# Optimization experiments

Measured on AMD Instinct MI355X. Metric: run time of the kernel, lower is better.

## Reference

```python
import jax, jax.numpy as jnp
import numpy as np

B, SD, SE = 4, 2048, 2048
HID, HID_ = 300, 512
N_HEADS = 8


def setup_inputs() -> dict:
    key = jax.random.key(0)
    ks = jax.random.split(key, 7)
    en = jax.random.normal(ks[0], (B, SE, HID), dtype=jnp.float32)
    de = jax.random.normal(ks[1], (B, SD, HID), dtype=jnp.float32)
    mask = jax.random.randint(ks[2], (1, 1, SD, SE), 0, 2).astype(jnp.bool_)
    WQ = jax.random.normal(ks[3], (HID, HID_), dtype=jnp.float32)
    WK = jax.random.normal(ks[4], (HID, HID_), dtype=jnp.float32)
    WV = jax.random.normal(ks[5], (HID, HID_), dtype=jnp.float32)
    WO = jax.random.normal(ks[6], (HID_, HID), dtype=jnp.float32)
    return {"en": en, "de": de, "mask": mask, "WQ": WQ, "WK": WK, "WV": WV, "WO": WO}


def reference(en, de, mask, WQ, WK, WV, WO):
    # Faithful to the torch module (dropout in eval mode => identity).
    d_k = de.shape[-1]  # NOTE: original scales by sqrt(hidden_dim)=sqrt(300), not head_dim
    b_d, s_d = de.shape[0], de.shape[1]
    b_e, s_e = en.shape[0], en.shape[1]
    # head axis is the LAST axis of the reshape (size 8), exactly as the original view/permute
    q = jnp.transpose((de @ WQ).reshape(b_d, s_d, -1, N_HEADS), (3, 0, 1, 2))  # [8,B,Sd,64]
    k = jnp.transpose((en @ WK).reshape(b_e, s_e, -1, N_HEADS), (3, 0, 2, 1))  # [8,B,64,Se]
    v = jnp.transpose((en @ WV).reshape(b_e, s_e, -1, N_HEADS), (3, 0, 1, 2))  # [8,B,Se,64]
    e = jnp.matmul(q, k) / jnp.sqrt(jnp.asarray(d_k, dtype=q.dtype))           # [8,B,Sd,Se]
    e = jnp.where(mask, jnp.asarray(-1e9, dtype=e.dtype), e)
    alpha = jax.nn.softmax(e, axis=3)
    head3 = jnp.matmul(alpha, v)                                               # [8,B,Sd,64]
    # torch.cat((head3[0],...,head3[7]), 2) == move head axis into feature concat order
    a = jnp.concatenate([head3[h] for h in range(N_HEADS)], axis=2)            # [B,Sd,512]
    return a @ WO                                                              # [B,Sd,300]
```

## Files before the change

kernel.cpp:

```cpp
#include <hip/hip_runtime.h>
#include <hip/hip_bf16.h>
#include <math.h>

#define B_      4
#define SD_     2048
#define SE_     2048
#define HIDIN   300
#define HIDMID  512
#define NH      8
#define DH      64
#define ESZ     ((size_t)4194304)
#define BUFB    24576

typedef __attribute__((ext_vector_type(8))) short          s16x8;
typedef __attribute__((ext_vector_type(8))) unsigned short u16x8;
typedef __attribute__((ext_vector_type(4))) unsigned short u16x4;
typedef __attribute__((ext_vector_type(4))) float          f32x4;

#define MFMA16 __builtin_amdgcn_mfma_f32_16x16x32_bf16

#define QSCALE  0.0832940411f
#define NEGL   -1.4426950e9f
#define DEFER_THR 24.0f

__device__ __forceinline__ unsigned short f2bf(float f) {
    unsigned int u = __float_as_uint(f);
    u += 0x7fffu + ((u >> 16) & 1u);
    return (unsigned short)(u >> 16);
}
__device__ __forceinline__ float bf2f(unsigned short s) {
    return __uint_as_float((unsigned int)s << 16);
}
__device__ __forceinline__ void gload16(const void* g, void* l) {
    __builtin_amdgcn_global_load_lds(
        (const __attribute__((address_space(1))) void*)g,
        (__attribute__((address_space(3))) void*)l, 16, 0, 0);
}

#define OF_QH   ((size_t)0)
#define OF_QL   (ESZ)
#define OF_KH   (2*ESZ)
#define OF_KL   (3*ESZ)
#define OF_VT   (4*ESZ)
#define OF_CA   (5*ESZ)
#define OF_CW   (OF_CA + 10485760)
#define OF_WOT  (OF_CW + 983040)

__global__ __launch_bounds__(256) void bias_kernel(const int* __restrict__ mask,
                                                   unsigned int* __restrict__ BiasT)
{
    const int idx = blockIdx.x * 256 + threadIdx.x;
    const int q = idx >> 5, tile = idx & 31;
    const int* __restrict__ mrow = mask + (size_t)q * SE_ + tile * 64;
    const unsigned int NEGB = (unsigned int)f2bf(NEGL);
    const int qblk = q >> 4, qlo = q & 15;
#pragma unroll
    for (int g = 0; g < 4; ++g) {
        unsigned int w[8];
#pragma unroll
        for (int sub = 0; sub < 4; ++sub) {
            const int4 mm = *(const int4*)(mrow + sub * 16 + g * 4);
            w[sub * 2]     = (mm.x ? NEGB : 0u) | ((mm.y ? NEGB : 0u) << 16);
            w[sub * 2 + 1] = (mm.z ? NEGB : 0u) | ((mm.w ? NEGB : 0u) << 16);
        }
        unsigned int* dst = BiasT +
            ((((size_t)qblk * 32 + tile) * 4 + g) * 16 + qlo) * 8;
        *(uint4*)dst       = make_uint4(w[0], w[1], w[2], w[3]);
        *(uint4*)(dst + 4) = make_uint4(w[4], w[5], w[6], w[7]);
    }
}

__global__ __launch_bounds__(256) void convA_kernel(
    const float* __restrict__ de, const float* __restrict__ en,
    unsigned short* __restrict__ CA)
{
    const int idx = blockIdx.x * 256 + threadIdx.x;
    const int mat = blockIdx.y;
    const float* __restrict__ A = mat ? en : de;
    unsigned short* __restrict__ H = CA + (size_t)mat * 5242880;
    unsigned short* __restrict__ L = H + 2621440;
    const int row = idx / 10, ch = idx - row * 10;
    float v[32];
    if (ch < 9) {
#pragma unroll
        for (int i = 0; i < 8; ++i) {
            const float4 f = *(const float4*)(A + (size_t)row * 300 + ch * 32 + i * 4);
            v[i*4+0] = f.x; v[i*4+1] = f.y; v[i*4+2] = f.z; v[i*4+3] = f.w;
        }
    } else {
#pragma unroll
        for (int i = 0; i < 32; ++i) {
            const int k = 288 + i;
            v[i] = (k < 300) ? A[(size_t)row * 300 + k] : 0.f;
        }
    }
    const int r128 = row & 127;
    const int xr = (r128 >> 1) & 3;
    const size_t tb = ((size_t)(row >> 7) * 10 + ch) * 4096 + r128 * 32;
#pragma unroll
    for (int sub = 0; sub < 4; ++sub) {
        const int slot = sub ^ xr;
        u16x8 hv, lv;
#pragma unroll
        for (int e = 0; e < 8; ++e) {
            const float f = v[sub * 8 + e];
            const unsigned short h = f2bf(f);
            hv[e] = h; lv[e] = f2bf(f - bf2f(h));
        }
        *(u16x8*)(H + tb + slot * 8) = hv;
        *(u16x8*)(L + tb + slot * 8) = lv;
    }
}

__global__ __launch_bounds__(256) void convW_kernel(
    const float* __restrict__ WQ, const float* __restrict__ WK,
    const float* __restrict__ WV, const float* __restrict__ WO,
    unsigned short* __restrict__ CW, unsigned short* __restrict__ WOT)
{
    const int idx = blockIdx.x * 256 + threadIdx.x;
    if (idx < 122880) {
        const int which = idx / 40960;
        const int rem = idx - which * 40960;
        const int k = rem >> 7;
        const int n0 = (rem & 127) * 4;
        const float* __restrict__ W = which == 0 ? WQ : (which == 1 ? WK : WV);
        unsigned short* __restrict__ H = CW + (size_t)which * 327680;
        unsigned short* __restrict__ L = H + 163840;
        const float sc = (which == 0) ? QSCALE : 1.f;
        float4 w = make_float4(0.f, 0.f, 0.f, 0.f);
        if (k < 300) w = *(const float4*)(W + (size_t)k * 512 + n0);
        const float wv4[4] = {w.x * sc, w.y * sc, w.z * sc, w.w * sc};
        const int ch = k >> 5, kk = k & 31;
#pragma unroll
        for (int j = 0; j < 4; ++j) {
            const int n = n0 + j, ntile = n >> 7, nr = n & 127;
            const size_t o = ((size_t)(ntile * 10 + ch) * 128 + nr) * 32
                           + (((kk >> 3) ^ ((nr >> 1) & 3)) << 3) + (kk & 7);
            const unsigned short h = f2bf(wv4[j]);
            H[o] = h; L[o] = f2bf(wv4[j] - bf2f(h));
        }
    } else {
        const int idx2 = idx - 122880;
        const int k = idx2 / 96, n4 = idx2 - k * 96;
        const int n0 = n4 * 4;
        float4 w = make_float4(0.f, 0.f, 0.f, 0.f);
        if (n0 < 300) w = *(const float4*)(WO + (size_t)k * 300 + n0);
        const float wv4[4] = {w.x, w.y, w.z, w.w};
        const int ch = k >> 5, kk = k & 31;
#pragma unroll
        for (int j = 0; j < 4; ++j) {
            const int n = n0 + j, ntile = n >> 7, nr = n & 127;
            const size_t o = ((size_t)(ntile * 16 + ch) * 128 + nr) * 32
                           + (((kk >> 3) ^ ((nr >> 1) & 3)) << 3) + (kk & 7);
            WOT[o] = f2bf(wv4[j]);
        }
    }
}

__global__ __launch_bounds__(256) void proj_mfma_kernel(
    const unsigned short* __restrict__ CA, const unsigned short* __restrict__ CW,
    unsigned short* __restrict__ Qh, unsigned short* __restrict__ Ql,
    unsigned short* __restrict__ KhT, unsigned short* __restrict__ KlT,
    unsigned short* __restrict__ VtT)
{
    const int stile = blockIdx.x, jtile = blockIdx.y, which = blockIdx.z;
    const int tid = threadIdx.x, wv = tid >> 6, lane = tid & 63;
    const int li = lane & 15, g = lane >> 4;
    const int wr = wv >> 1, wc = wv & 1;

    __shared__ __align__(16) char LBp[65536];

    const unsigned short* __restrict__ pAh =
        CA + (size_t)(which ? 1 : 0) * 5242880 + (size_t)stile * 40960 + tid * 8;
    const unsigned short* __restrict__ pAl = pAh + 2621440;
    const unsigned short* __restrict__ pWh =
        CW + (size_t)which * 327680 + (size_t)jtile * 40960 + tid * 8;
    const unsigned short* __restrict__ pWl = pWh + 163840;

#define STAGEP(ch, bofs) {                                                    \
        char* db = LBp + (bofs) + wv * 1024;                                  \
        const size_t co = (size_t)(ch) * 4096;                                \
        gload16(pAh + co,        db);                                         \
        gload16(pAh + co + 2048, db + 4096);                                  \
        gload16(pAl + co,        db + 8192);                                  \
        gload16(pAl + co + 2048, db + 12288);                                 \
        gload16(pWh + co,        db + 16384);                                 \
        gload16(pWh + co + 2048, db + 20480);                                 \
        gload16(pWl + co,        db + 24576);                                 \
        gload16(pWl + co + 2048, db + 28672);                                 \
    }

    int offA[4], offW[4];
#pragma unroll
    for (int ssub = 0; ssub < 4; ++ssub) {
        const int r = wr * 64 + ssub * 16 + li;
        offA[ssub] = r * 64 + ((g ^ ((r >> 1) & 3)) << 4);
    }
#pragma unroll
    for (int jsub = 0; jsub < 4; ++jsub) {
        const int n = wc * 64 + jsub * 16 + li;
        offW[jsub] = n * 64 + ((g ^ ((n >> 1) & 3)) << 4);
    }

    f32x4 acc[4][4];
#pragma unroll
    for (int i = 0; i < 4; ++i)
#pragma unroll
        for (int j = 0; j < 4; ++j) acc[i][j] = (f32x4){0.f, 0.f, 0.f, 0.f};

    STAGEP(0, 0)
    __syncthreads();

#pragma unroll 1
    for (int ch = 0; ch < 10; ++ch) {
        const int bofs = (ch & 1) * 32768;
        if (ch < 9) STAGEP(ch + 1, bofs ^ 32768)
        const char* bp = LBp + bofs;
        s16x8 ah[4], al[4], wh[4], wl[4];
#pragma unroll
        for (int ssub = 0; ssub < 4; ++ssub) {
            ah[ssub] = *(const s16x8*)(bp + offA[ssub]);
            al[ssub] = *(const s16x8*)(bp + 8192 + offA[ssub]);
        }
#pragma unroll
        for (int jsub = 0; jsub < 4; ++jsub) {
            wh[jsub] = *(const s16x8*)(bp + 16384 + offW[jsub]);
            wl[jsub] = *(const s16x8*)(bp + 24576 + offW[jsub]);
        }
        __builtin_amdgcn_s_setprio(1);
#pragma unroll
        for (int ssub = 0; ssub < 4; ++ssub)
#pragma unroll
            for (int jsub = 0; jsub < 4; ++jsub) {
                acc[ssub][jsub] = MFMA16(ah[ssub], wh[jsub], acc[ssub][jsub], 0, 0, 0);
                acc[ssub][jsub] = MFMA16(ah[ssub], wl[jsub], acc[ssub][jsub], 0, 0, 0);
                acc[ssub][jsub] = MFMA16(al[ssub], wh[jsub], acc[ssub][jsub], 0, 0, 0);
            }
        __builtin_amdgcn_s_setprio(0);
        __syncthreads();
    }
#undef STAGEP

    const int jgbase = jtile * 128 + wc * 64 + li;
    const int sbase0 = stile * 128 + wr * 64 + 4 * g;
#pragma unroll
    for (int jsub = 0; jsub < 4; ++jsub) {
        const int jgg = jgbase + jsub * 16;
        const int d = jgg >> 3, hh = jgg & 7;
#pragma unroll
        for (int ssub = 0; ssub < 4; ++ssub) {
            const f32x4 v = acc[ssub][jsub];
            const int sg0 = sbase0 + ssub * 16;
            const int bbv = sg0 >> 11;
            const int bhn = bbv * 8 + hh;
            const int sl0 = sg0 & 2047;
            if (which == 0) {
                const size_t o = ((size_t)bhn * 2048 + sl0) * 64 + d;
#pragma unroll
                for (int r = 0; r < 4; ++r) {
                    const float val = v[r];
                    const unsigned short hi = f2bf(val);
                    Qh[o + r * 64] = hi;
                    Ql[o + r * 64] = f2bf(val - bf2f(hi));
                }
            } else if (which == 1) {
                const int tile = sl0 >> 6, tt0 = sl0 & 63;
                const size_t tb = ((size_t)(bhn * 32 + tile)) << 12;
#pragma unroll
                for (int r = 0; r < 4; ++r) {
                    const int tt = tt0 + r;
                    const size_t o = tb + tt * 64 + (((d >> 3) ^ (tt & 7)) << 3) + (d & 7);
                    const float val = v[r];
                    const unsigned short hi = f2bf(val);
                    KhT[o] = hi;
                    KlT[o] = f2bf(val - bf2f(hi));
                }
            } else {
                const int tile = sl0 >> 6, tin0 = sl0 & 63;
                const size_t tb = ((size_t)(bhn * 32 + tile)) << 12;
                const int blk = tin0 >> 5, gg2 = (tin0 >> 2) & 3, half = (tin0 >> 4) & 1;
                const size_t o = tb + (size_t)d * 64
                               + ((((blk << 2) | gg2) ^ (d & 7)) << 3) + half * 4;
                u16x4 pk;
#pragma unroll
                for (int r = 0; r < 4; ++r) pk[r] = f2bf(v[r]);
                *(u16x4*)(VtT + o) = pk;
            }
        }
    }
}

__global__ __launch_bounds__(256, 2) void attn_mfma_kernel(
    const unsigned short* __restrict__ Qh, const unsigned short* __restrict__ Ql,
    const unsigned short* __restrict__ KhT, const unsigned short* __restrict__ KlT,
    const unsigned short* __restrict__ VtT, const unsigned int* __restrict__ BiasT,
    unsigned short* __restrict__ AOb)
{
    const int lin = blockIdx.x + 16 * blockIdx.y;
    const int qt = (lin >> 3) & 15;
    const int bh = (lin & 7) + ((lin >> 7) << 3);
    const int bb = bh >> 3, hh = bh & 7;
    const int tid = threadIdx.x;
    const int wv = tid >> 6, lane = tid & 63;
    const int g = lane >> 4, li = lane & 15;
    const int q0r = qt * 128 + wv * 16 + li;

    __shared__ __align__(16) char LB[3 * BUFB];

    const size_t qoff = ((size_t)bh * SD_ + q0r) * DH + 8 * g;
    const s16x8 qh0_0 = *(const s16x8*)(Qh + qoff);
    const s16x8 qh1_0 = *(const s16x8*)(Qh + qoff + 32);
    const s16x8 ql0_0 = *(const s16x8*)(Ql + qoff);
    const s16x8 ql1_0 = *(const s16x8*)(Ql + qoff + 32);
    const s16x8 qh0_1 = *(const s16x8*)(Qh + qoff + 4096);
    const s16x8 qh1_1 = *(const s16x8*)(Qh + qoff + 4128);
    const s16x8 ql0_1 = *(const s16x8*)(Ql + qoff + 4096);
    const s16x8 ql1_1 = *(const s16x8*)(Ql + qoff + 4128);

    const unsigned short* __restrict__ sKh = KhT + ((size_t)bh << 17) + tid * 8;
    const unsigned short* __restrict__ sKl = KlT + ((size_t)bh << 17) + tid * 8;
    const unsigned short* __restrict__ sVt = VtT + ((size_t)bh << 17) + tid * 8;

    const int base0 = li * 128 + ((g ^ (li & 7)) << 4);
    const int base1 = li * 128 + (((4 + g) ^ (li & 7)) << 4);

    const size_t bb0 = ((((size_t)(qt * 8 + 0 * 4 + wv)) * 32) * 4 + g) * 16 * 8 + li * 8;
    const size_t bb1 = ((((size_t)(qt * 8 + 1 * 4 + wv)) * 32) * 4 + g) * 16 * 8 + li * 8;
#define BIASLOAD(T, R0A, R0B, R1A, R1B) {                                     \
        const uint4* p0 = (const uint4*)(BiasT + bb0 + (size_t)(T) * 512);    \
        R0A = p0[0]; R0B = p0[1];                                             \
        const uint4* p1 = (const uint4*)(BiasT + bb1 + (size_t)(T) * 512);    \
        R1A = p1[0]; R1B = p1[1];                                             \
    }

#define STAGE(tile, boff)                                                     \
    {                                                                         \
        char* db = LB + (boff) + wv * 1024;                                   \
        const size_t toff = (size_t)(tile) << 12;                             \
        gload16(sKh + toff,        db);                                       \
        gload16(sKh + toff + 2048, db + 4096);                                \
        gload16(sKl + toff,        db + 8192);                                \
        gload16(sKl + toff + 2048, db + 12288);                               \
        gload16(sVt + toff,        db + 16384);                               \
        gload16(sVt + toff + 2048, db + 20480);                               \
    }

    float m0 = -INFINITY, m1 = -INFINITY;
    f32x4 O0[4], O1[4], lacc0, lacc1;
#pragma unroll
    for (int i = 0; i < 4; ++i) {
        O0[i] = (f32x4){0.f, 0.f, 0.f, 0.f};
        O1[i] = (f32x4){0.f, 0.f, 0.f, 0.f};
    }
    lacc0 = (f32x4){0.f, 0.f, 0.f, 0.f};
    lacc1 = (f32x4){0.f, 0.f, 0.f, 0.f};

    s16x8 ones;
#pragma unroll
    for (int i = 0; i < 8; ++i) ones[i] = (short)0x3F80;

    uint4 cA0, cA1, cB0, cB1;
    uint4 nA0, nA1, nB0, nB1;

    STAGE(0, 0)
    BIASLOAD(0, cA0, cA1, cB0, cB1)
    STAGE(1, BUFB)
    asm volatile("s_waitcnt vmcnt(6)" ::: "memory");
    __builtin_amdgcn_s_barrier();
    __builtin_amdgcn_sched_barrier(0);

    int cc = 0, cs = 2 * BUFB;

#define UNPK(W, S, sub, cbase)                                                \
        S[sub][cbase]     = __uint_as_float((W) << 16);                       \
        S[sub][cbase + 1] = __uint_as_float((W) & 0xFFFF0000u);

#define ITER(IT, C0A, C0B, C1A, C1B, N0A, N0B, N1A, N1B)                      \
    {                                                                         \
        f32x4 s0[4], s1[4];                                                   \
        UNPK(C0A.x, s0, 0, 0) UNPK(C0A.y, s0, 0, 2)                           \
        UNPK(C0A.z, s0, 1, 0) UNPK(C0A.w, s0, 1, 2)                           \
        UNPK(C0B.x, s0, 2, 0) UNPK(C0B.y, s0, 2, 2)                           \
        UNPK(C0B.z, s0, 3, 0) UNPK(C0B.w, s0, 3, 2)                           \
        UNPK(C1A.x, s1, 0, 0) UNPK(C1A.y, s1, 0, 2)                           \
        UNPK(C1A.z, s1, 1, 0) UNPK(C1A.w, s1, 1, 2)                           \
        UNPK(C1B.x, s1, 2, 0) UNPK(C1B.y, s1, 2, 2)                           \
        UNPK(C1B.z, s1, 3, 0) UNPK(C1B.w, s1, 3, 2)                           \
        BIASLOAD(((IT) + 1) & 31, N0A, N0B, N1A, N1B)                         \
        __builtin_amdgcn_s_setprio(1);                                        \
        _Pragma("unroll")                                                     \
        for (int sub = 0; sub < 4; ++sub) {                                   \
            const s16x8 kh0 = *(const s16x8*)(LB + cc + base0 + sub * 2048);  \
            const s16x8 kh1 = *(const s16x8*)(LB + cc + base1 + sub * 2048);  \
            const s16x8 kl0 = *(const s16x8*)(LB + cc + base0 + 8192 + sub * 2048); \
            const s16x8 kl1 = *(const s16x8*)(LB + cc + base1 + 8192 + sub * 2048); \
            s0[sub] = MFMA16(kh0, qh0_0, s0[sub], 0, 0, 0);                   \
            s0[sub] = MFMA16(kh0, ql0_0, s0[sub], 0, 0, 0);                   \
            s0[sub] = MFMA16(kl0, qh0_0, s0[sub], 0, 0, 0);                   \
            s0[sub] = MFMA16(kh1, qh1_0, s0[sub], 0, 0, 0);                   \
            s0[sub] = MFMA16(kh1, ql1_0, s0[sub], 0, 0, 0);                   \
            s0[sub] = MFMA16(kl1, qh1_0, s0[sub], 0, 0, 0);                   \
            s1[sub] = MFMA16(kh0, qh0_1, s1[sub], 0, 0, 0);                   \
            s1[sub] = MFMA16(kh0, ql0_1, s1[sub], 0, 0, 0);                   \
            s1[sub] = MFMA16(kl0, qh0_1, s1[sub], 0, 0, 0);                   \
            s1[sub] = MFMA16(kh1, qh1_1, s1[sub], 0, 0, 0);                   \
            s1[sub] = MFMA16(kh1, ql1_1, s1[sub], 0, 0, 0);                   \
            s1[sub] = MFMA16(kl1, qh1_1, s1[sub], 0, 0, 0);                   \
        }                                                                     \
        __builtin_amdgcn_s_setprio(0);                                        \
        float t0, t1;                                                         \
        {                                                                     \
            float a = fmaxf(s0[0][0], fmaxf(s0[0][1], s0[0][2]));             \
            float b = fmaxf(s0[0][3], fmaxf(s0[1][0], s0[1][1]));             \
            float c = fmaxf(s0[1][2], fmaxf(s0[1][3], s0[2][0]));             \
            float d = fmaxf(s0[2][1], fmaxf(s0[2][2], s0[2][3]));             \
            float e = fmaxf(s0[3][0], fmaxf(s0[3][1], s0[3][2]));             \
            t0 = fmaxf(fmaxf(a, fmaxf(b, c)), fmaxf(s0[3][3], fmaxf(d, e)));  \
        }                                                                     \
        {                                                                     \
            float a = fmaxf(s1[0][0], fmaxf(s1[0][1], s1[0][2]));             \
            float b = fmaxf(s1[0][3], fmaxf(s1[1][0], s1[1][1]));             \
            float c = fmaxf(s1[1][2], fmaxf(s1[1][3], s1[2][0]));             \
            float d = fmaxf(s1[2][1], fmaxf(s1[2][2], s1[2][3]));             \
            float e = fmaxf(s1[3][0], fmaxf(s1[3][1], s1[3][2]));             \
            t1 = fmaxf(fmaxf(a, fmaxf(b, c)), fmaxf(s1[3][3], fmaxf(d, e)));  \
        }                                                                     \
        const int okd = (t0 <= m0 + DEFER_THR) && (t1 <= m1 + DEFER_THR);     \
        if (!__all(okd)) {                                                    \
            float r0 = fmaxf(t0, __shfl_xor(t0, 16));                         \
            r0 = fmaxf(r0, __shfl_xor(r0, 32));                               \
            float r1 = fmaxf(t1, __shfl_xor(t1, 16));                         \
            r1 = fmaxf(r1, __shfl_xor(r1, 32));                               \
            const float mn0 = fmaxf(m0, r0), mn1 = fmaxf(m1, r1);             \
            const float sc0 = exp2f(m0 - mn0), sc1 = exp2f(m1 - mn1);         \
            m0 = mn0; m1 = mn1;                                               \
            _Pragma("unroll")                                                 \
            for (int i = 0; i < 4; ++i) { O0[i] *= sc0; O1[i] *= sc1; }       \
            lacc0 *= sc0; lacc1 *= sc1;                                       \
        }                                                                     \
        _Pragma("unroll")                                                     \
        for (int sub = 0; sub < 4; ++sub)                                     \
            _Pragma("unroll")                                                 \
            for (int c = 0; c < 4; ++c) {                                     \
                s0[sub][c] = exp2f(s0[sub][c] - m0);                          \
                s1[sub][c] = exp2f(s1[sub][c] - m1);                          \
            }                                                                 \
        union { s16x8 v; unsigned int w[4]; } P00, P10, P01, P11;             \
        asm("v_cvt_pk_bf16_f32 %0, %1, %2" : "=v"(P00.w[0]) : "v"(s0[0][0]), "v"(s0[0][1])); \
        asm("v_cvt_pk_bf16_f32 %0, %1, %2" : "=v"(P00.w[1]) : "v"(s0[0][2]), "v"(s0[0][3])); \
        asm("v_cvt_pk_bf16_f32 %0, %1, %2" : "=v"(P00.w[2]) : "v"(s0[1][0]), "v"(s0[1][1])); \
        asm("v_cvt_pk_bf16_f32 %0, %1, %2" : "=v"(P00.w[3]) : "v"(s0[1][2]), "v"(s0[1][3])); \
        asm("v_cvt_pk_bf16_f32 %0, %1, %2" : "=v"(P10.w[0]) : "v"(s0[2][0]), "v"(s0[2][1])); \
        asm("v_cvt_pk_bf16_f32 %0, %1, %2" : "=v"(P10.w[1]) : "v"(s0[2][2]), "v"(s0[2][3])); \
        asm("v_cvt_pk_bf16_f32 %0, %1, %2" : "=v"(P10.w[2]) : "v"(s0[3][0]), "v"(s0[3][1])); \
        asm("v_cvt_pk_bf16_f32 %0, %1, %2" : "=v"(P10.w[3]) : "v"(s0[3][2]), "v"(s0[3][3])); \
        asm("v_cvt_pk_bf16_f32 %0, %1, %2" : "=v"(P01.w[0]) : "v"(s1[0][0]), "v"(s1[0][1])); \
        asm("v_cvt_pk_bf16_f32 %0, %1, %2" : "=v"(P01.w[1]) : "v"(s1[0][2]), "v"(s1[0][3])); \
        asm("v_cvt_pk_bf16_f32 %0, %1, %2" : "=v"(P01.w[2]) : "v"(s1[1][0]), "v"(s1[1][1])); \
        asm("v_cvt_pk_bf16_f32 %0, %1, %2" : "=v"(P01.w[3]) : "v"(s1[1][2]), "v"(s1[1][3])); \
        asm("v_cvt_pk_bf16_f32 %0, %1, %2" : "=v"(P11.w[0]) : "v"(s1[2][0]), "v"(s1[2][1])); \
        asm("v_cvt_pk_bf16_f32 %0, %1, %2" : "=v"(P11.w[1]) : "v"(s1[2][2]), "v"(s1[2][3])); \
        asm("v_cvt_pk_bf16_f32 %0, %1, %2" : "=v"(P11.w[2]) : "v"(s1[3][0]), "v"(s1[3][1])); \
        asm("v_cvt_pk_bf16_f32 %0, %1, %2" : "=v"(P11.w[3]) : "v"(s1[3][2]), "v"(s1[3][3])); \
        __builtin_amdgcn_s_setprio(1);                                        \
        _Pragma("unroll")                                                     \
        for (int dsub = 0; dsub < 4; ++dsub) {                                \
            const s16x8 vf0 = *(const s16x8*)(LB + cc + base0 + 16384 + dsub * 2048); \
            const s16x8 vf1 = *(const s16x8*)(LB + cc + base1 + 16384 + dsub * 2048); \
            O0[dsub] = MFMA16(vf0, P00.v, O0[dsub], 0, 0, 0);                 \
            O0[dsub] = MFMA16(vf1, P10.v, O0[dsub], 0, 0, 0);                 \
            O1[dsub] = MFMA16(vf0, P01.v, O1[dsub], 0, 0, 0);                 \
            O1[dsub] = MFMA16(vf1, P11.v, O1[dsub], 0, 0, 0);                 \
        }                                                                     \
        lacc0 = MFMA16(ones, P00.v, lacc0, 0, 0, 0);                          \
        lacc0 = MFMA16(ones, P10.v, lacc0, 0, 0, 0);                          \
        lacc1 = MFMA16(ones, P01.v, lacc1, 0, 0, 0);                          \
        lacc1 = MFMA16(ones, P11.v, lacc1, 0, 0, 0);                          \
        __builtin_amdgcn_s_setprio(0);                                        \
        STAGE(((IT) + 2) & 31, cs)                                            \
        asm volatile("s_waitcnt vmcnt(6)" ::: "memory");                      \
        __builtin_amdgcn_s_barrier();                                         \
        __builtin_amdgcn_sched_barrier(0);                                    \
        cc += BUFB; if (cc == 3 * BUFB) cc = 0;                               \
        cs += BUFB; if (cs == 3 * BUFB) cs = 0;                               \
    }

#pragma unroll 1
    for (int itp = 0; itp < 32; itp += 2) {
        ITER(itp,     cA0, cA1, cB0, cB1, nA0, nA1, nB0, nB1)
        ITER(itp + 1, nA0, nA1, nB0, nB1, cA0, cA1, cB0, cB1)
    }

#pragma unroll
    for (int qs = 0; qs < 2; ++qs) {
        const float rl = 1.f / (qs ? lacc1[0] : lacc0[0]);
        const f32x4* Oq = qs ? O1 : O0;
        const int row = bb * 2048 + qt * 128 + qs * 64 + wv * 16 + li;
        const int r128 = row & 127;
        const int xr = (r128 >> 1) & 3;
        unsigned short* __restrict__ ab = AOb + ((size_t)(row >> 7)) * 65536
                                        + r128 * 32 + (g & 1) * 4;
#pragma unroll
        for (int dsub = 0; dsub < 4; ++dsub) {
            const f32x4 o = Oq[dsub] * rl;
            const int ch = hh * 2 + (dsub >> 1);
            const int slot = ((dsub & 1) * 2 + (g >> 1)) ^ xr;
            u16x4 pk;
#pragma unroll
            for (int c = 0; c < 4; ++c) pk[c] = f2bf(o[c]);
            *(u16x4*)(ab + (size_t)ch * 4096 + slot * 8) = pk;
        }
    }
#undef STAGE
#undef BIASLOAD
#undef UNPK
#undef ITER
}

__global__ __launch_bounds__(256) void epi_mfma_kernel(
    const unsigned short* __restrict__ AOb, const unsigned short* __restrict__ WOT,
    float* __restrict__ out)
{
    const int stile = blockIdx.x, jtile = blockIdx.y;
    const int tid = threadIdx.x, wv = tid >> 6, lane = tid & 63;
    const int li = lane & 15, g = lane >> 4;

    __shared__ __align__(16) char LBe[24576];

    const unsigned short* __restrict__ pA =
        AOb + (size_t)(stile >> 1) * 65536 + (stile & 1) * 2048 + tid * 8;
    const unsigned short* __restrict__ pW = WOT + (size_t)jtile * 65536 + tid * 8;

#define STAGEE(ch, bofs) {                                                    \
        char* dbA = LBe + (bofs) + wv * 1024;                                 \
        const size_t co = (size_t)(ch) * 4096;                                \
        gload16(pA + co,        dbA);                                         \
        gload16(pW + co,        dbA + 4096);                                  \
        gload16(pW + co + 2048, dbA + 8192);                                  \
    }

    int offA[4], offW[2];
#pragma unroll
    for (int ssub = 0; ssub < 4; ++ssub) {
        const int r = ssub * 16 + li;
        offA[ssub] = r * 64 + ((g ^ ((r >> 1) & 3)) << 4);
    }
#pragma unroll
    for (int jsub = 0; jsub < 2; ++jsub) {
        const int n = wv * 32 + jsub * 16 + li;
        offW[jsub] = 4096 + n * 64 + ((g ^ ((n >> 1) & 3)) << 4);
    }

    f32x4 acc[4][2];
#pragma unroll
    for (int i = 0; i < 4; ++i)
#pragma unroll
        for (int j = 0; j < 2; ++j) acc[i][j] = (f32x4){0.f, 0.f, 0.f, 0.f};

    STAGEE(0, 0)
    __syncthreads();

#pragma unroll 1
    for (int ch = 0; ch < 16; ++ch) {
        const int bofs = (ch & 1) * 12288;
        if (ch < 15) STAGEE(ch + 1, bofs ^ 12288)
        const char* bp = LBe + bofs;
        s16x8 ah[4], wh[2];
#pragma unroll
        for (int ssub = 0; ssub < 4; ++ssub)
            ah[ssub] = *(const s16x8*)(bp + offA[ssub]);
#pragma unroll
        for (int jsub = 0; jsub < 2; ++jsub)
            wh[jsub] = *(const s16x8*)(bp + offW[jsub]);
        __builtin_amdgcn_s_setprio(1);
#pragma unroll
        for (int ssub = 0; ssub < 4; ++ssub)
#pragma unroll
            for (int jsub = 0; jsub < 2; ++jsub)
                acc[ssub][jsub] = MFMA16(ah[ssub], wh[jsub], acc[ssub][jsub], 0, 0, 0);
        __builtin_amdgcn_s_setprio(0);
        __syncthreads();
    }
#undef STAGEE

    const int nbase = jtile * 128 + wv * 32 + li;
    const int rbase = stile * 64 + 4 * g;
#pragma unroll
    for (int jsub = 0; jsub < 2; ++jsub) {
        const int o = nbase + jsub * 16;
        if (o < HIDIN) {
#pragma unroll
            for (int ssub = 0; ssub < 4; ++ssub) {
                const f32x4 v = acc[ssub][jsub];
                const int r0 = rbase + ssub * 16;
#pragma unroll
                for (int r = 0; r < 4; ++r)
                    out[(size_t)(r0 + r) * HIDIN + o] = v[r];
            }
        }
    }
}

extern "C" void kernel_launch(void* const* d_in, const int* in_sizes, int n_in,
                              void* d_out, int out_size, void* d_ws, size_t ws_size,
                              hipStream_t stream)
{
    const float* en  = (const float*)d_in[0];
    const float* de  = (const float*)d_in[1];
    const int*   mask = (const int*)d_in[2];
    const float* WQ  = (const float*)d_in[3];
    const float* WK  = (const float*)d_in[4];
    const float* WV  = (const float*)d_in[5];
    const float* WO  = (const float*)d_in[6];
    float* out = (float*)d_out;

    unsigned short* ws2 = (unsigned short*)d_ws;
    unsigned short* Qh  = ws2 + OF_QH;
    unsigned short* Ql  = ws2 + OF_QL;
    unsigned short* KhT = ws2 + OF_KH;
    unsigned short* KlT = ws2 + OF_KL;
    unsigned short* VtT = ws2 + OF_VT;
    unsigned short* CA  = ws2 + OF_CA;
    unsigned short* CW  = ws2 + OF_CW;
    unsigned short* WOT = ws2 + OF_WOT;
    unsigned short* AOb = CA;
    unsigned int*  BiasT = (unsigned int*)(CA + 4194304);

    convA_kernel<<<dim3(320, 2), 256, 0, stream>>>(de, en, CA);
    convW_kernel<<<dim3(672), 256, 0, stream>>>(WQ, WK, WV, WO, CW, WOT);
    proj_mfma_kernel<<<dim3(64, 4, 3), 256, 0, stream>>>(CA, CW, Qh, Ql, KhT, KlT, VtT);
    bias_kernel<<<dim3(256), 256, 0, stream>>>(mask, BiasT);
    attn_mfma_kernel<<<dim3(16, 32), 256, 0, stream>>>(Qh, Ql, KhT, KlT, VtT, BiasT, AOb);
    epi_mfma_kernel<<<dim3(128, 3), 256, 0, stream>>>(AOb, WOT, out);
}
```

Before: 187.8 us.

## Split attention block into 8 waves of one query tile each, skip V lo-split

The attention kernel moves from 4 waves handling two 16-row query groups each to 8 waves handling one group each, with 512 threads per block. Each thread now stages one K-hi, K-lo and V chunk per tile instead of two, and the wait count is adjusted to match. The goal is to halve per-wave register pressure and work, which raises latency hiding and occupancy. Separately, the V projection drops its low-part bf16 split and the two correction MFMAs, since V is consumed only in bf16. This removes matmul work and loads but slightly lowers V precision, and the larger blocks add barrier cost across more waves.

```diff
diff --git a/kernel.cpp b/kernel.cpp
--- a/kernel.cpp
+++ b/kernel.cpp
@@ -137,7 +137,8 @@
             const size_t o = ((size_t)(ntile * 10 + ch) * 128 + nr) * 32
                            + (((kk >> 3) ^ ((nr >> 1) & 3)) << 3) + (kk & 7);
             const unsigned short h = f2bf(wv4[j]);
-            H[o] = h; L[o] = f2bf(wv4[j] - bf2f(h));
+            H[o] = h;
+            if (which < 2) L[o] = f2bf(wv4[j] - bf2f(h));
         }
     } else {
         const int idx2 = idx - 122880;
@@ -182,12 +183,16 @@
         const size_t co = (size_t)(ch) * 4096;                                \
         gload16(pAh + co,        db);                                         \
         gload16(pAh + co + 2048, db + 4096);                                  \
-        gload16(pAl + co,        db + 8192);                                  \
-        gload16(pAl + co + 2048, db + 12288);                                 \
+        if (which < 2) {                                                      \
+            gload16(pAl + co,        db + 8192);                              \
+            gload16(pAl + co + 2048, db + 12288);                             \
+        }                                                                     \
         gload16(pWh + co,        db + 16384);                                 \
         gload16(pWh + co + 2048, db + 20480);                                 \
-        gload16(pWl + co,        db + 24576);                                 \
-        gload16(pWl + co + 2048, db + 28672);                                 \
+        if (which < 2) {                                                      \
+            gload16(pWl + co,        db + 24576);                             \
+            gload16(pWl + co + 2048, db + 28672);                             \
+        }                                                                     \
     }
 
     int offA[4], offW[4];
@@ -220,12 +225,12 @@
 #pragma unroll
         for (int ssub = 0; ssub < 4; ++ssub) {
             ah[ssub] = *(const s16x8*)(bp + offA[ssub]);
-            al[ssub] = *(const s16x8*)(bp + 8192 + offA[ssub]);
+            if (which < 2) al[ssub] = *(const s16x8*)(bp + 8192 + offA[ssub]);
         }
 #pragma unroll
         for (int jsub = 0; jsub < 4; ++jsub) {
             wh[jsub] = *(const s16x8*)(bp + 16384 + offW[jsub]);
-            wl[jsub] = *(const s16x8*)(bp + 24576 + offW[jsub]);
+            if (which < 2) wl[jsub] = *(const s16x8*)(bp + 24576 + offW[jsub]);
         }
         __builtin_amdgcn_s_setprio(1);
 #pragma unroll
@@ -233,8 +238,10 @@
 #pragma unroll
             for (int jsub = 0; jsub < 4; ++jsub) {
                 acc[ssub][jsub] = MFMA16(ah[ssub], wh[jsub], acc[ssub][jsub], 0, 0, 0);
-                acc[ssub][jsub] = MFMA16(ah[ssub], wl[jsub], acc[ssub][jsub], 0, 0, 0);
-                acc[ssub][jsub] = MFMA16(al[ssub], wh[jsub], acc[ssub][jsub], 0, 0, 0);
+                if (which < 2) {
+                    acc[ssub][jsub] = MFMA16(ah[ssub], wl[jsub], acc[ssub][jsub], 0, 0, 0);
+                    acc[ssub][jsub] = MFMA16(al[ssub], wh[jsub], acc[ssub][jsub], 0, 0, 0);
+                }
             }
         __builtin_amdgcn_s_setprio(0);
         __syncthreads();
@@ -290,7 +297,7 @@
     }
 }
 
-__global__ __launch_bounds__(256, 2) void attn_mfma_kernel(
+__global__ __launch_bounds__(512, 4) void attn_mfma_kernel(
     const unsigned short* __restrict__ Qh, const unsigned short* __restrict__ Ql,
     const unsigned short* __restrict__ KhT, const unsigned short* __restrict__ KlT,
     const unsigned short* __restrict__ VtT, const unsigned int* __restrict__ BiasT,
@@ -303,19 +310,15 @@
     const int tid = threadIdx.x;
     const int wv = tid >> 6, lane = tid & 63;
     const int g = lane >> 4, li = lane & 15;
-    const int q0r = qt * 128 + wv * 16 + li;
+    const int q = qt * 128 + wv * 16 + li;
 
     __shared__ __align__(16) char LB[3 * BUFB];
 
-    const size_t qoff = ((size_t)bh * SD_ + q0r) * DH + 8 * g;
-    const s16x8 qh0_0 = *(const s16x8*)(Qh + qoff);
-    const s16x8 qh1_0 = *(const s16x8*)(Qh + qoff + 32);
-    const s16x8 ql0_0 = *(const s16x8*)(Ql + qoff);
-    const s16x8 ql1_0 = *(const s16x8*)(Ql + qoff + 32);
-    const s16x8 qh0_1 = *(const s16x8*)(Qh + qoff + 4096);
-    const s16x8 qh1_1 = *(const s16x8*)(Qh + qoff + 4128);
-    const s16x8 ql0_1 = *(const s16x8*)(Ql + qoff + 4096);
-    const s16x8 ql1_1 = *(const s16x8*)(Ql + qoff + 4128);
+    const size_t qoff = ((size_t)bh * SD_ + q) * DH + 8 * g;
+    const s16x8 qh0 = *(const s16x8*)(Qh + qoff);
+    const s16x8 qh1 = *(const s16x8*)(Qh + qoff + 32);
+    const s16x8 ql0 = *(const s16x8*)(Ql + qoff);
+    const s16x8 ql1 = *(const s16x8*)(Ql + qoff + 32);
 
     const unsigned short* __restrict__ sKh = KhT + ((size_t)bh << 17) + tid * 8;
     const unsigned short* __restrict__ sKl = KlT + ((size_t)bh << 17) + tid * 8;
@@ -324,69 +327,47 @@
     const int base0 = li * 128 + ((g ^ (li & 7)) << 4);
     const int base1 = li * 128 + (((4 + g) ^ (li & 7)) << 4);
 
-    const size_t bb0 = ((((size_t)(qt * 8 + 0 * 4 + wv)) * 32) * 4 + g) * 16 * 8 + li * 8;
-    const size_t bb1 = ((((size_t)(qt * 8 + 1 * 4 + wv)) * 32) * 4 + g) * 16 * 8 + li * 8;
-#define BIASLOAD(T, R0A, R0B, R1A, R1B) {                                     \
-        const uint4* p0 = (const uint4*)(BiasT + bb0 + (size_t)(T) * 512);    \
-        R0A = p0[0]; R0B = p0[1];                                             \
-        const uint4* p1 = (const uint4*)(BiasT + bb1 + (size_t)(T) * 512);    \
-        R1A = p1[0]; R1B = p1[1];                                             \
+    const size_t bbase = (size_t)(qt * 8 + wv) * 16384 + g * 128 + li * 8;
+
+#define BIASLOAD(T, RA, RB) {                                                 \
+        const uint4* p = (const uint4*)(BiasT + bbase + (size_t)(T) * 512);   \
+        RA = p[0]; RB = p[1];                                                 \
     }
 
 #define STAGE(tile, boff)                                                     \
     {                                                                         \
         char* db = LB + (boff) + wv * 1024;                                   \
         const size_t toff = (size_t)(tile) << 12;                             \
-        gload16(sKh + toff,        db);                                       \
-        gload16(sKh + toff + 2048, db + 4096);                                \
-        gload16(sKl + toff,        db + 8192);                                \
-        gload16(sKl + toff + 2048, db + 12288);                               \
-        gload16(sVt + toff,        db + 16384);                               \
-        gload16(sVt + toff + 2048, db + 20480);                               \
-    }
-
-    float m0 = -INFINITY, m1 = -INFINITY;
-    f32x4 O0[4], O1[4], lacc0, lacc1;
-#pragma unroll
-    for (int i = 0; i < 4; ++i) {
-        O0[i] = (f32x4){0.f, 0.f, 0.f, 0.f};
-        O1[i] = (f32x4){0.f, 0.f, 0.f, 0.f};
-    }
-    lacc0 = (f32x4){0.f, 0.f, 0.f, 0.f};
-    lacc1 = (f32x4){0.f, 0.f, 0.f, 0.f};
+        gload16(sKh + toff, db);                                              \
+        gload16(sKl + toff, db + 8192);                                       \
+        gload16(sVt + toff, db + 16384);                                      \
+    }
+
+    float m = -INFINITY;
+    f32x4 O[4], lacc;
+#pragma unroll
+    for (int i = 0; i < 4; ++i) O[i] = (f32x4){0.f, 0.f, 0.f, 0.f};
+    lacc = (f32x4){0.f, 0.f, 0.f, 0.f};
 
     s16x8 ones;
 #pragma unroll
     for (int i = 0; i < 8; ++i) ones[i] = (short)0x3F80;
 
-    uint4 cA0, cA1, cB0, cB1;
-    uint4 nA0, nA1, nB0, nB1;
-
-    STAGE(0, 0)
-    BIASLOAD(0, cA0, cA1, cB0, cB1)
-    STAGE(1, BUFB)
-    asm volatile("s_waitcnt vmcnt(6)" ::: "memory");
-    __builtin_amdgcn_s_barrier();
-    __builtin_amdgcn_sched_barrier(0);
-
-    int cc = 0, cs = 2 * BUFB;
+    uint4 cBA, cBB, nBA, nBB;
 
 #define UNPK(W, S, sub, cbase)                                                \
         S[sub][cbase]     = __uint_as_float((W) << 16);                       \
         S[sub][cbase + 1] = __uint_as_float((W) & 0xFFFF0000u);
 
-#define ITER(IT, C0A, C0B, C1A, C1B, N0A, N0B, N1A, N1B)                      \
+#define ITER(IT, CBA_, CBB_, NBA_, NBB_)                                      \
     {                                                                         \
-        f32x4 s0[4], s1[4];                                                   \
-        UNPK(C0A.x, s0, 0, 0) UNPK(C0A.y, s0, 0, 2)                           \
-        UNPK(C0A.z, s0, 1, 0) UNPK(C0A.w, s0, 1, 2)                           \
-        UNPK(C0B.x, s0, 2, 0) UNPK(C0B.y, s0, 2, 2)                           \
-        UNPK(C0B.z, s0, 3, 0) UNPK(C0B.w, s0, 3, 2)                           \
-        UNPK(C1A.x, s1, 0, 0) UNPK(C1A.y, s1, 0, 2)                           \
-        UNPK(C1A.z, s1, 1, 0) UNPK(C1A.w, s1, 1, 2)                           \
-        UNPK(C1B.x, s1, 2, 0) UNPK(C1B.y, s1, 2, 2)                           \
-        UNPK(C1B.z, s1, 3, 0) UNPK(C1B.w, s1, 3, 2)                           \
-        BIASLOAD(((IT) + 1) & 31, N0A, N0B, N1A, N1B)                         \
+        BIASLOAD(((IT) + 1) & 31, NBA_, NBB_)                                 \
+        STAGE(((IT) + 2) & 31, cs)                                            \
+        f32x4 s[4];                                                           \
+        UNPK(CBA_.x, s, 0, 0) UNPK(CBA_.y, s, 0, 2)                           \
+        UNPK(CBA_.z, s, 1, 0) UNPK(CBA_.w, s, 1, 2)                           \
+        UNPK(CBB_.x, s, 2, 0) UNPK(CBB_.y, s, 2, 2)                           \
+        UNPK(CBB_.z, s, 3, 0) UNPK(CBB_.w, s, 3, 2)                           \
         __builtin_amdgcn_s_setprio(1);                                        \
         _Pragma("unroll")                                                     \
         for (int sub = 0; sub < 4; ++sub) {                                   \
@@ -394,122 +375,93 @@
             const s16x8 kh1 = *(const s16x8*)(LB + cc + base1 + sub * 2048);  \
             const s16x8 kl0 = *(const s16x8*)(LB + cc + base0 + 8192 + sub * 2048); \
             const s16x8 kl1 = *(const s16x8*)(LB + cc + base1 + 8192 + sub * 2048); \
-            s0[sub] = MFMA16(kh0, qh0_0, s0[sub], 0, 0, 0);                   \
-            s0[sub] = MFMA16(kh0, ql0_0, s0[sub], 0, 0, 0);                   \
-            s0[sub] = MFMA16(kl0, qh0_0, s0[sub], 0, 0, 0);                   \
-            s0[sub] = MFMA16(kh1, qh1_0, s0[sub], 0, 0, 0);                   \
-            s0[sub] = MFMA16(kh1, ql1_0, s0[sub], 0, 0, 0);                   \
-            s0[sub] = MFMA16(kl1, qh1_0, s0[sub], 0, 0, 0);                   \
-            s1[sub] = MFMA16(kh0, qh0_1, s1[sub], 0, 0, 0);                   \
-            s1[sub] = MFMA16(kh0, ql0_1, s1[sub], 0, 0, 0);                   \
-            s1[sub] = MFMA16(kl0, qh0_1, s1[sub], 0, 0, 0);                   \
-            s1[sub] = MFMA16(kh1, qh1_1, s1[sub], 0, 0, 0);                   \
-            s1[sub] = MFMA16(kh1, ql1_1, s1[sub], 0, 0, 0);                   \
-            s1[sub] = MFMA16(kl1, qh1_1, s1[sub], 0, 0, 0);                   \
+            s[sub] = MFMA16(kh0, qh0, s[sub], 0, 0, 0);                       \
+            s[sub] = MFMA16(kh0, ql0, s[sub], 0, 0, 0);                       \
+            s[sub] = MFMA16(kl0, qh0, s[sub], 0, 0, 0);                       \
+            s[sub] = MFMA16(kh1, qh1, s[sub], 0, 0, 0);                       \
+            s[sub] = MFMA16(kh1, ql1, s[sub], 0, 0, 0);                       \
+            s[sub] = MFMA16(kl1, qh1, s[sub], 0, 0, 0);                       \
         }                                                                     \
         __builtin_amdgcn_s_setprio(0);                                        \
-        float t0, t1;                                                         \
-        {                                                                     \
-            float a = fmaxf(s0[0][0], fmaxf(s0[0][1], s0[0][2]));             \
-            float b = fmaxf(s0[0][3], fmaxf(s0[1][0], s0[1][1]));             \
-            float c = fmaxf(s0[1][2], fmaxf(s0[1][3], s0[2][0]));             \
-            float d = fmaxf(s0[2][1], fmaxf(s0[2][2], s0[2][3]));             \
-            float e = fmaxf(s0[3][0], fmaxf(s0[3][1], s0[3][2]));             \
-            t0 = fmaxf(fmaxf(a, fmaxf(b, c)), fmaxf(s0[3][3], fmaxf(d, e)));  \
-        }                                                                     \
-        {                                                                     \
-            float a = fmaxf(s1[0][0], fmaxf(s1[0][1], s1[0][2]));             \
-            float b = fmaxf(s1[0][3], fmaxf(s1[1][0], s1[1][1]));             \
-            float c = fmaxf(s1[1][2], fmaxf(s1[1][3], s1[2][0]));             \
-            float d = fmaxf(s1[2][1], fmaxf(s1[2][2], s1[2][3]));             \
-            float e = fmaxf(s1[3][0], fmaxf(s1[3][1], s1[3][2]));             \
-            t1 = fmaxf(fmaxf(a, fmaxf(b, c)), fmaxf(s1[3][3], fmaxf(d, e)));  \
-        }                                                                     \
-        const int okd = (t0 <= m0 + DEFER_THR) && (t1 <= m1 + DEFER_THR);     \
-        if (!__all(okd)) {                                                    \
-            float r0 = fmaxf(t0, __shfl_xor(t0, 16));                         \
-            r0 = fmaxf(r0, __shfl_xor(r0, 32));                               \
-            float r1 = fmaxf(t1, __shfl_xor(t1, 16));                         \
-            r1 = fmaxf(r1, __shfl_xor(r1, 32));                               \
-            const float mn0 = fmaxf(m0, r0), mn1 = fmaxf(m1, r1);             \
-            const float sc0 = exp2f(m0 - mn0), sc1 = exp2f(m1 - mn1);         \
-            m0 = mn0; m1 = mn1;                                               \
+        float x0 = fmaxf(fmaxf(s[0][0], s[0][1]), s[0][2]);                   \
+        float x1 = fmaxf(fmaxf(s[0][3], s[1][0]), s[1][1]);                   \
+        float x2 = fmaxf(fmaxf(s[1][2], s[1][3]), s[2][0]);                   \
+        float x3 = fmaxf(fmaxf(s[2][1], s[2][2]), s[2][3]);                   \
+        float x4 = fmaxf(fmaxf(s[3][0], s[3][1]), s[3][2]);                   \
+        float tmax = fmaxf(fmaxf(fmaxf(x0, x1), fmaxf(x2, x3)),               \
+                           fmaxf(x4, s[3][3]));                               \
+        if (!__all(tmax <= m + DEFER_THR)) {                                  \
+            float r = fmaxf(tmax, __shfl_xor(tmax, 16));                      \
+            r = fmaxf(r, __shfl_xor(r, 32));                                  \
+            const float mn  = fmaxf(m, r);                                    \
+            const float scl = exp2f(m - mn);                                  \
+            m = mn;                                                           \
             _Pragma("unroll")                                                 \
-            for (int i = 0; i < 4; ++i) { O0[i] *= sc0; O1[i] *= sc1; }       \
-            lacc0 *= sc0; lacc1 *= sc1;                                       \
+            for (int i = 0; i < 4; ++i) O[i] *= scl;                          \
+            lacc *= scl;                                                      \
         }                                                                     \
         _Pragma("unroll")                                                     \
         for (int sub = 0; sub < 4; ++sub)                                     \
             _Pragma("unroll")                                                 \
-            for (int c = 0; c < 4; ++c) {                                     \
-                s0[sub][c] = exp2f(s0[sub][c] - m0);                          \
-                s1[sub][c] = exp2f(s1[sub][c] - m1);                          \
-            }                                                                 \
-        union { s16x8 v; unsigned int w[4]; } P00, P10, P01, P11;             \
-        asm("v_cvt_pk_bf16_f32 %0, %1, %2" : "=v"(P00.w[0]) : "v"(s0[0][0]), "v"(s0[0][1])); \
-        asm("v_cvt_pk_bf16_f32 %0, %1, %2" : "=v"(P00.w[1]) : "v"(s0[0][2]), "v"(s0[0][3])); \
-        asm("v_cvt_pk_bf16_f32 %0, %1, %2" : "=v"(P00.w[2]) : "v"(s0[1][0]), "v"(s0[1][1])); \
-        asm("v_cvt_pk_bf16_f32 %0, %1, %2" : "=v"(P00.w[3]) : "v"(s0[1][2]), "v"(s0[1][3])); \
-        asm("v_cvt_pk_bf16_f32 %0, %1, %2" : "=v"(P10.w[0]) : "v"(s0[2][0]), "v"(s0[2][1])); \
-        asm("v_cvt_pk_bf16_f32 %0, %1, %2" : "=v"(P10.w[1]) : "v"(s0[2][2]), "v"(s0[2][3])); \
-        asm("v_cvt_pk_bf16_f32 %0, %1, %2" : "=v"(P10.w[2]) : "v"(s0[3][0]), "v"(s0[3][1])); \
-        asm("v_cvt_pk_bf16_f32 %0, %1, %2" : "=v"(P10.w[3]) : "v"(s0[3][2]), "v"(s0[3][3])); \
-        asm("v_cvt_pk_bf16_f32 %0, %1, %2" : "=v"(P01.w[0]) : "v"(s1[0][0]), "v"(s1[0][1])); \
-        asm("v_cvt_pk_bf16_f32 %0, %1, %2" : "=v"(P01.w[1]) : "v"(s1[0][2]), "v"(s1[0][3])); \
-        asm("v_cvt_pk_bf16_f32 %0, %1, %2" : "=v"(P01.w[2]) : "v"(s1[1][0]), "v"(s1[1][1])); \
-        asm("v_cvt_pk_bf16_f32 %0, %1, %2" : "=v"(P01.w[3]) : "v"(s1[1][2]), "v"(s1[1][3])); \
-        asm("v_cvt_pk_bf16_f32 %0, %1, %2" : "=v"(P11.w[0]) : "v"(s1[2][0]), "v"(s1[2][1])); \
-        asm("v_cvt_pk_bf16_f32 %0, %1, %2" : "=v"(P11.w[1]) : "v"(s1[2][2]), "v"(s1[2][3])); \
-        asm("v_cvt_pk_bf16_f32 %0, %1, %2" : "=v"(P11.w[2]) : "v"(s1[3][0]), "v"(s1[3][1])); \
-        asm("v_cvt_pk_bf16_f32 %0, %1, %2" : "=v"(P11.w[3]) : "v"(s1[3][2]), "v"(s1[3][3])); \
+            for (int c = 0; c < 4; ++c)                                       \
+                s[sub][c] = exp2f(s[sub][c] - m);                             \
+        union { s16x8 v; unsigned int w[4]; } P0, P1;                         \
+        asm("v_cvt_pk_bf16_f32 %0, %1, %2" : "=v"(P0.w[0]) : "v"(s[0][0]), "v"(s[0][1])); \
+        asm("v_cvt_pk_bf16_f32 %0, %1, %2" : "=v"(P0.w[1]) : "v"(s[0][2]), "v"(s[0][3])); \
+        asm("v_cvt_pk_bf16_f32 %0, %1, %2" : "=v"(P0.w[2]) : "v"(s[1][0]), "v"(s[1][1])); \
+        asm("v_cvt_pk_bf16_f32 %0, %1, %2" : "=v"(P0.w[3]) : "v"(s[1][2]), "v"(s[1][3])); \
+        asm("v_cvt_pk_bf16_f32 %0, %1, %2" : "=v"(P1.w[0]) : "v"(s[2][0]), "v"(s[2][1])); \
+        asm("v_cvt_pk_bf16_f32 %0, %1, %2" : "=v"(P1.w[1]) : "v"(s[2][2]), "v"(s[2][3])); \
+        asm("v_cvt_pk_bf16_f32 %0, %1, %2" : "=v"(P1.w[2]) : "v"(s[3][0]), "v"(s[3][1])); \
+        asm("v_cvt_pk_bf16_f32 %0, %1, %2" : "=v"(P1.w[3]) : "v"(s[3][2]), "v"(s[3][3])); \
         __builtin_amdgcn_s_setprio(1);                                        \
         _Pragma("unroll")                                                     \
         for (int dsub = 0; dsub < 4; ++dsub) {                                \
             const s16x8 vf0 = *(const s16x8*)(LB + cc + base0 + 16384 + dsub * 2048); \
             const s16x8 vf1 = *(const s16x8*)(LB + cc + base1 + 16384 + dsub * 2048); \
-            O0[dsub] = MFMA16(vf0, P00.v, O0[dsub], 0, 0, 0);                 \
-            O0[dsub] = MFMA16(vf1, P10.v, O0[dsub], 0, 0, 0);                 \
-            O1[dsub] = MFMA16(vf0, P01.v, O1[dsub], 0, 0, 0);                 \
-            O1[dsub] = MFMA16(vf1, P11.v, O1[dsub], 0, 0, 0);                 \
+            O[dsub] = MFMA16(vf0, P0.v, O[dsub], 0, 0, 0);                    \
+            O[dsub] = MFMA16(vf1, P1.v, O[dsub], 0, 0, 0);                    \
         }                                                                     \
-        lacc0 = MFMA16(ones, P00.v, lacc0, 0, 0, 0);                          \
-        lacc0 = MFMA16(ones, P10.v, lacc0, 0, 0, 0);                          \
-        lacc1 = MFMA16(ones, P01.v, lacc1, 0, 0, 0);                          \
-        lacc1 = MFMA16(ones, P11.v, lacc1, 0, 0, 0);                          \
+        lacc = MFMA16(ones, P0.v, lacc, 0, 0, 0);                             \
+        lacc = MFMA16(ones, P1.v, lacc, 0, 0, 0);                             \
         __builtin_amdgcn_s_setprio(0);                                        \
-        STAGE(((IT) + 2) & 31, cs)                                            \
-        asm volatile("s_waitcnt vmcnt(6)" ::: "memory");                      \
+        asm volatile("s_waitcnt vmcnt(3)" ::: "memory");                      \
         __builtin_amdgcn_s_barrier();                                         \
         __builtin_amdgcn_sched_barrier(0);                                    \
         cc += BUFB; if (cc == 3 * BUFB) cc = 0;                               \
         cs += BUFB; if (cs == 3 * BUFB) cs = 0;                               \
     }
 
+    int cc = 0, cs = 2 * BUFB;
+
+    BIASLOAD(0, cBA, cBB)
+    STAGE(0, 0)
+    STAGE(1, BUFB)
+    asm volatile("s_waitcnt vmcnt(3)" ::: "memory");
+    __builtin_amdgcn_s_barrier();
+    __builtin_amdgcn_sched_barrier(0);
+
 #pragma unroll 1
-    for (int itp = 0; itp < 32; itp += 2) {
-        ITER(itp,     cA0, cA1, cB0, cB1, nA0, nA1, nB0, nB1)
-        ITER(itp + 1, nA0, nA1, nB0, nB1, cA0, cA1, cB0, cB1)
-    }
-
-#pragma unroll
-    for (int qs = 0; qs < 2; ++qs) {
-        const float rl = 1.f / (qs ? lacc1[0] : lacc0[0]);
-        const f32x4* Oq = qs ? O1 : O0;
-        const int row = bb * 2048 + qt * 128 + qs * 64 + wv * 16 + li;
-        const int r128 = row & 127;
-        const int xr = (r128 >> 1) & 3;
-        unsigned short* __restrict__ ab = AOb + ((size_t)(row >> 7)) * 65536
-                                        + r128 * 32 + (g & 1) * 4;
-#pragma unroll
-        for (int dsub = 0; dsub < 4; ++dsub) {
-            const f32x4 o = Oq[dsub] * rl;
-            const int ch = hh * 2 + (dsub >> 1);
-            const int slot = ((dsub & 1) * 2 + (g >> 1)) ^ xr;
-            u16x4 pk;
-#pragma unroll
-            for (int c = 0; c < 4; ++c) pk[c] = f2bf(o[c]);
-            *(u16x4*)(ab + (size_t)ch * 4096 + slot * 8) = pk;
-        }
+    for (int it = 0; it < 32; it += 2) {
+        ITER(it,     cBA, cBB, nBA, nBB)
+        ITER(it + 1, nBA, nBB, cBA, cBB)
+    }
+
+    const float rl = 1.f / lacc[0];
+    const int row = bb * 2048 + q;
+    const int r128 = row & 127;
+    const int xr = (r128 >> 1) & 3;
+    unsigned short* __restrict__ ab = AOb + ((size_t)(row >> 7)) * 65536
+                                    + r128 * 32 + (g & 1) * 4;
+#pragma unroll
+    for (int dsub = 0; dsub < 4; ++dsub) {
+        const f32x4 o = O[dsub] * rl;
+        const int ch = hh * 2 + (dsub >> 1);
+        const int slot = ((dsub & 1) * 2 + (g >> 1)) ^ xr;
+        u16x4 pk;
+#pragma unroll
+        for (int c = 0; c < 4; ++c) pk[c] = f2bf(o[c]);
+        *(u16x4*)(ab + (size_t)ch * 4096 + slot * 8) = pk;
     }
 #undef STAGE
 #undef BIASLOAD
@@ -630,6 +582,6 @@
     convW_kernel<<<dim3(672), 256, 0, stream>>>(WQ, WK, WV, WO, CW, WOT);
     proj_mfma_kernel<<<dim3(64, 4, 3), 256, 0, stream>>>(CA, CW, Qh, Ql, KhT, KlT, VtT);
     bias_kernel<<<dim3(256), 256, 0, stream>>>(mask, BiasT);
-    attn_mfma_kernel<<<dim3(16, 32), 256, 0, stream>>>(Qh, Ql, KhT, KlT, VtT, BiasT, AOb);
+    attn_mfma_kernel<<<dim3(16, 32), 512, 0, stream>>>(Qh, Ql, KhT, KlT, VtT, BiasT, AOb);
     epi_mfma_kernel<<<dim3(128, 3), 256, 0, stream>>>(AOb, WOT, out);
 }
```

Result: no change. 186.0 us (-0.9%).
